# Kernel tuning notes

Measured on AMD Instinct MI355X. Metric: run time of the kernel, lower is better.

Reference implementation:

```python
import jax, jax.numpy as jnp
import numpy as np
import math

NLAT, NLON, LMAX, MMAX = 512, 1024, 50, 50
CHUNK = 8192  # grid chunk for brute-force 3-NN (keeps dist matrix ~134MB)


def _cc_nodes_weights(n):
    """Clenshaw-Curtis nodes theta_j = pi*j/(n-1) and weights for int_{-1}^{1} f(cos t)."""
    N = n - 1
    t = np.pi * np.arange(n) / N
    K = N // 2
    k = np.arange(1, K + 1)
    b = np.where(2 * k == N, 1.0, 2.0)
    S = np.cos(2.0 * np.outer(t, k)) @ (b / (4.0 * k ** 2 - 1.0))
    c = np.full(n, 2.0); c[0] = c[-1] = 1.0
    w = (c / N) * (1.0 - S)
    return t, w


def _legendre(lmax, mmax, theta):
    """Orthonormalized associated Legendre P[l, m, j] = N_lm P_l^m(cos theta_j)."""
    ct, st = np.cos(theta), np.sin(theta)
    P = np.zeros((lmax, mmax, theta.shape[0]))
    P[0, 0] = math.sqrt(1.0 / (4.0 * math.pi))
    for m in range(1, mmax):
        P[m, m] = -math.sqrt((2 * m + 1) / (2.0 * m)) * st * P[m - 1, m - 1]
    for m in range(mmax):
        if m + 1 < lmax:
            P[m + 1, m] = math.sqrt(2 * m + 3) * ct * P[m, m]
        for l in range(m + 2, lmax):
            a = math.sqrt((4.0 * l * l - 1.0) / (l * l - m * m))
            bb = math.sqrt(((l - 1.0) ** 2 - m * m) / (4.0 * (l - 1.0) ** 2 - 1.0))
            P[l, m] = a * (ct * P[l - 1, m] - bb * P[l - 2, m])
    return P

_THETA, _WQ_np = _cc_nodes_weights(NLAT)
_PLM = jnp.asarray(_legendre(LMAX, MMAX, _THETA), jnp.float32)   # (lmax, mmax, nlat)
_WQ = jnp.asarray(_WQ_np, jnp.float32)                            # (nlat,)

# equiangular target grid from __init__: theta in [0, pi), phi in [-pi, pi)
_gi, _gj = np.meshgrid(np.arange(0, 512), np.arange(-512, 512), indexing='ij')
_GRID = jnp.asarray(np.stack([_gi.ravel(), _gj.ravel()], -1).astype(np.float32) / 512.0 * np.pi)  # (M, 2)


def to_spherical(coords):
    """coords (B,N,3) -> (r (B,N), angles (B,N,2)) with azimuth already shifted by -pi."""
    x, y, z = coords[..., 0], coords[..., 1], coords[..., 2]
    r = jnp.sqrt(x * x + y * y + z * z)
    nyz = jnp.sqrt(y * y + z * z)          # tril-norm chain reduces to (r, ||(y,z)||, |z|)
    phi1 = jnp.arccos(x / r)
    base = jnp.arccos(y / nyz)
    phi2 = jnp.where(z < 0, 2.0 * jnp.pi - base, base)
    sph = jnp.stack([phi1, phi2 - jnp.pi], -1)  # forward() subtracts pi from azimuth
    return r, sph


def three_nn(grid, pts):
    """grid (M,2), pts (B,N,2) -> squared dists (B,M,3), idx (B,M,3) of 3 nearest cloud points."""
    gch = grid.reshape(-1, CHUNK, 2)

    def per_batch(p):
        def f(g):
            d2 = jnp.sum((g[:, None, :] - p[None, :, :]) ** 2, -1)  # (CHUNK, N)
            nd, idx = jax.lax.top_k(-d2, 3)
            return -nd, idx
        d, i = jax.lax.map(f, gch)
        return d.reshape(-1, 3), i.reshape(-1, 3)

    return jax.vmap(per_batch)(pts)


def real_sht(f):
    """f (B, nlat, nlon) -> complex coeffs (B, lmax, mmax)."""
    F = jnp.fft.rfft(f, axis=-1)[:, :, :MMAX] * (2.0 * jnp.pi / NLON)  # (B, nlat, mmax)
    Fw = F * _WQ[None, :, None]
    return jnp.einsum('bkm,lmk->blm', Fw, _PLM)


def _branch(pc):
    r, sph = to_spherical(pc)
    dist, idx = three_nn(_GRID, sph)
    w = dist / jnp.sum(dist, -1, keepdims=True)                  # faithful: dist/sum, not 1/dist
    rg = jax.vmap(lambda rr, ii: rr[ii])(r, idx)                 # (B, M, 3)
    interp = jnp.sum(rg * w, -1).reshape(-1, NLAT, NLON)
    return real_sht(interp)


def setup_inputs() -> dict:
    key = jax.random.key(0)
    k1, k2 = jax.random.split(key)
    pred = jax.random.normal(k1, (2, 2048, 3), dtype=jnp.float32)
    target = jax.random.normal(k2, (2, 2048, 3), dtype=jnp.float32)
    return {"pred": pred, "target": target}


def reference(pred, target):
    cp = _branch(pred)
    ct = _branch(target)
    return jnp.mean((cp.real - ct.real) ** 2)
```

## Files before the change

### kernel.cpp

```cpp
#include <hip/hip_runtime.h>
#include <math.h>

#define NLAT 512
#define NLON 1024
#define LMAX 50
#define MMAX 50
#define NPTS 2048
#define NIMG 4
#define M_GRID (NLAT * NLON)

#define NBT 32
#define NBP 64
#define NBINS (NBT * NBP)
#define NPAIR (2 * LMAX * MMAX)
#define NTRI  (LMAX * (LMAX + 1) / 2)

#define PI_F     3.14159274101257324e0f
#define TWO_PI_F 6.28318548202514648e0f
#define WB       (PI_F / 32.0f)
#define INV_WB   (32.0f / PI_F)

__global__ __launch_bounds__(256) void k_setup_bin(const float* __restrict__ pred,
                                                   const float* __restrict__ targ,
                                                   float* __restrict__ wq,
                                                   double* __restrict__ costab,
                                                   float* __restrict__ plm,
                                                   float4* __restrict__ spts_g,
                                                   unsigned short* __restrict__ bstart_g,
                                                   double* __restrict__ acc,
                                                   int* __restrict__ counter) {
    if (blockIdx.x < 128) {
        int tid = blockIdx.x * 256 + threadIdx.x;
        if (tid == 0) { acc[0] = 0.0; counter[0] = 0; }

        {
            int j = blockIdx.x * 4 + (threadIdx.x >> 6);
            int lane = threadIdx.x & 63;
            double t = M_PI * (double)j / 511.0;
            double S = 0.0;
            for (int k = lane + 1; k <= 255; k += 64) {
                S += cos(2.0 * t * (double)k) * (2.0 / (4.0 * (double)k * k - 1.0));
            }
            for (int off = 32; off > 0; off >>= 1) S += __shfl_down(S, off);
            if (lane == 0) {
                double c = (j == 0 || j == 511) ? 1.0 : 2.0;
                wq[j] = (float)((c / 511.0) * (1.0 - S));
            }
        }
        if (tid < 1024) {
            costab[tid] = cos(2.0 * M_PI * (double)tid / 1024.0);
        }
        if (blockIdx.x < 100) {
            __shared__ double fa[MMAX];
            __shared__ double al[LMAX], bl[LMAX];
            int m = blockIdx.x >> 1;
            int t = threadIdx.x;
            if (t >= 1 && t < MMAX) {
                fa[t] = -sqrt((2.0 * t + 1.0) / (2.0 * t));
            }
            if (t >= m + 2 && t < LMAX) {
                double ll = (double)t, mm = (double)m, lm1 = (double)(t - 1);
                al[t] = sqrt((4.0 * ll * ll - 1.0) / (ll * ll - mm * mm));
                bl[t] = sqrt((lm1 * lm1 - mm * mm) / (4.0 * lm1 * lm1 - 1.0));
            }
            __syncthreads();
            int k = ((blockIdx.x & 1) << 8) + t;
            double theta = M_PI * (double)k / 511.0;
            double ct = cos(theta), st = sin(theta);
            double pmm = sqrt(1.0 / (4.0 * M_PI));
            for (int i = 1; i <= m; ++i) {
                pmm = fa[i] * st * pmm;
            }
            plm[((size_t)m * MMAX + m) * 512 + k] = (float)pmm;
            if (m + 1 < LMAX) {
                double pm1 = sqrt(2.0 * m + 3.0) * ct * pmm;
                plm[((size_t)(m + 1) * MMAX + m) * 512 + k] = (float)pm1;
                double pm2 = pmm;
                for (int l = m + 2; l < LMAX; ++l) {
                    double p = al[l] * (ct * pm1 - bl[l] * pm2);
                    plm[((size_t)l * MMAX + m) * 512 + k] = (float)p;
                    pm2 = pm1; pm1 = p;
                }
            }
        }
        return;
    }

    int img = blockIdx.x - 128;
    int branch = img >> 1, b = img & 1;
    const float* src = (branch ? targ : pred) + (size_t)b * NPTS * 3;
    __shared__ float sth[NPTS], sphi[NPTS], srr[NPTS];
    __shared__ int cnt[NBINS];
    __shared__ int bstart[NBINS];
    __shared__ int partial[256];
    __shared__ int binid[NPTS];
    int tid = threadIdx.x;

    for (int i = tid; i < NBINS; i += 256) cnt[i] = 0;
    for (int i = tid; i < NPTS; i += 256) {
        float x = src[3 * i], y = src[3 * i + 1], z = src[3 * i + 2];
        float r = sqrtf(x * x + y * y + z * z);
        float nyz = sqrtf(y * y + z * z);
        float phi1 = acosf(x / r);
        float base = acosf(y / nyz);
        float phi2 = (z < 0.0f) ? (TWO_PI_F - base) : base;
        sth[i] = phi1; sphi[i] = phi2 - PI_F; srr[i] = r;
    }
    __syncthreads();
    for (int i = tid; i < NPTS; i += 256) {
        int bt = min(max((int)(sth[i] * INV_WB), 0), NBT - 1);
        int bp = min(max((int)((sphi[i] + PI_F) * INV_WB), 0), NBP - 1);
        int bn = bt * NBP + bp;
        binid[i] = bn;
        atomicAdd(&cnt[bn], 1);
    }
    __syncthreads();
    int base = tid * 8, s = 0;
    #pragma unroll
    for (int j = 0; j < 8; ++j) s += cnt[base + j];
    partial[tid] = s;
    __syncthreads();
    for (int offs = 1; offs < 256; offs <<= 1) {
        int v = (tid >= offs) ? partial[tid - offs] : 0;
        __syncthreads();
        partial[tid] += v;
        __syncthreads();
    }
    int run = (tid == 0) ? 0 : partial[tid - 1];
    #pragma unroll
    for (int j = 0; j < 8; ++j) { bstart[base + j] = run; run += cnt[base + j]; }
    __syncthreads();
    unsigned short* bsg = bstart_g + (size_t)img * (NBINS + 1);
    for (int i = tid; i < NBINS; i += 256) {
        bsg[i] = (unsigned short)bstart[i];
        cnt[i] = bstart[i];
    }
    if (tid == 0) bsg[NBINS] = (unsigned short)NPTS;
    __syncthreads();
    float4* sg = spts_g + (size_t)img * NPTS;
    for (int i = tid; i < NPTS; i += 256) {
        int bn = binid[i];
        int pos = atomicAdd(&cnt[bn], 1);
        sg[pos] = make_float4(sth[i], sphi[i], srr[i], 0.0f);
    }
}

struct Top3 {
    float d0, d1, d2, r0, r1, r2;
    __device__ void init() { d0 = d1 = d2 = 1e30f; r0 = r1 = r2 = 0.0f; }
    __device__ void ins(float d, float rv) {
        bool c2 = d < d2, c1 = d < d1, c0 = d < d0;
        d2 = c1 ? d1 : (c2 ? d : d2);   r2 = c1 ? r1 : (c2 ? rv : r2);
        d1 = c0 ? d0 : (c1 ? d : d1);   r1 = c0 ? r0 : (c1 ? rv : r1);
        d0 = c0 ? d : d0;               r0 = c0 ? rv : r0;
    }
    __device__ float out() const {
        return (d0 * r0 + d1 * r1 + d2 * r2) / (d0 + d1 + d2);
    }
};

__global__ __launch_bounds__(512, 4) void k_nn(const float4* __restrict__ spts_g,
                                               const unsigned short* __restrict__ bstart_g,
                                               float* __restrict__ interp) {
    __shared__ float4 spts[NPTS];
    __shared__ unsigned short sstart[NBINS + 1];
    int bid = blockIdx.x;
    int img = bid >> 8;
    int blk = bid & 255;
    const float4* sg = spts_g + (size_t)img * NPTS;
    const unsigned short* bsg = bstart_g + (size_t)img * (NBINS + 1);
    int tid = threadIdx.x;
    for (int i = tid; i < NPTS; i += 512) spts[i] = sg[i];
    for (int i = tid; i < NBINS + 1; i += 512) sstart[i] = bsg[i];
    __syncthreads();

    int w = tid >> 6, lane = tid & 63;
    int patch = blk * 8 + w;
    int pi = patch >> 6, pj = patch & 63;
    int qi = lane >> 2, qj0 = (lane & 3) * 4;
    int gi = pi * 16 + qi;
    int gj0 = pj * 16 + qj0;
    float gt  = (float)gi * (1.0f / 512.0f) * PI_F;
    float gp0 = (float)(gj0     - 512) * (1.0f / 512.0f) * PI_F;
    float gp1 = (float)(gj0 + 1 - 512) * (1.0f / 512.0f) * PI_F;
    float gp2 = (float)(gj0 + 2 - 512) * (1.0f / 512.0f) * PI_F;
    float gp3 = (float)(gj0 + 3 - 512) * (1.0f / 512.0f) * PI_F;
    int qbt  = min(max((int)(gt * INV_WB), 0), NBT - 1);
    int qbp0 = min(max((int)((gp0 + PI_F) * INV_WB), 0), NBP - 1);
    int qbp3 = min(max((int)((gp3 + PI_F) * INV_WB), 0), NBP - 1);
    int bt0 = __shfl(qbt, 0), bt1 = __shfl(qbt, 63);
    int bp0 = __shfl(qbp0, 0), bp1 = __shfl(qbp3, 63);

    Top3 qA, qB, qC, qD;
    qA.init(); qB.init(); qC.init(); qD.init();

    auto scan_span = [&](int t, int p0, int p1) {
        int s = sstart[t * NBP + p0], e = sstart[t * NBP + p1 + 1];
        #pragma unroll 2
        for (int i = s; i < e; ++i) {
            float4 pt = spts[i];
            float dx  = gt - pt.x;
            float dxx = dx * dx;
            float dy0 = gp0 - pt.y;
            float dy1 = gp1 - pt.y;
            float dy2 = gp2 - pt.y;
            float dy3 = gp3 - pt.y;
            float dA  = fmaf(dy0, dy0, dxx);
            float dB  = fmaf(dy1, dy1, dxx);
            float dC  = fmaf(dy2, dy2, dxx);
            float dD  = fmaf(dy3, dy3, dxx);
            if (__any(dA < qA.d2 || dB < qB.d2)) {
                qA.ins(dA, pt.z);
                qB.ins(dB, pt.z);
            }
            if (__any(dC < qC.d2 || dD < qD.d2)) {
                qC.ins(dC, pt.z);
                qD.ins(dD, pt.z);
            }
        }
    };

    for (int t = bt0; t <= bt1; ++t) scan_span(t, bp0, bp1);
    for (int r = 1; r <= 70; ++r) {
        if (r >= 2) {
            float bnd = (float)(r - 1) * WB * 0.999f;
            float b2 = bnd * bnd;
            if (__all(b2 > qA.d2 && b2 > qB.d2 && b2 > qC.d2 && b2 > qD.d2)) break;
        }
        int tlo = bt0 - r, thi = bt1 + r, plo = bp0 - r, phi = bp1 + r;
        int cplo = max(plo, 0), cphi = min(phi, NBP - 1);
        if (tlo >= 0)       scan_span(tlo, cplo, cphi);
        if (thi <= NBT - 1) scan_span(thi, cplo, cphi);
        int ctlo = max(tlo + 1, 0), cthi = min(thi - 1, NBT - 1);
        if (plo >= 0)       for (int t = ctlo; t <= cthi; ++t) scan_span(t, plo, plo);
        if (phi <= NBP - 1) for (int t = ctlo; t <= cthi; ++t) scan_span(t, phi, phi);
        if (tlo <= 0 && thi >= NBT - 1 && plo <= 0 && phi >= NBP - 1) break;
    }
    float4 outv = make_float4(qA.out(), qB.out(), qC.out(), qD.out());
    *(float4*)&interp[(size_t)img * M_GRID + (size_t)gi * NLON + gj0] = outv;
}

__global__ __launch_bounds__(512) void k_dft(const float* __restrict__ interp,
                                             const double* __restrict__ costab,
                                             const float* __restrict__ wq,
                                             double* __restrict__ ediff) {
    __shared__ double sdf[NLON];
    __shared__ double sct[NLON];
    __shared__ double ge[320];
    __shared__ double go[320];
    int bid = blockIdx.x;
    int b = bid >> 9, k = bid & 511;
    const float* rowp = interp + (size_t)b * M_GRID + (size_t)k * NLON;
    const float* rowt = interp + (size_t)(2 + b) * M_GRID + (size_t)k * NLON;
    int tid = threadIdx.x;
    for (int i = tid; i < NLON; i += 512) {
        sdf[i] = (double)rowp[i] - (double)rowt[i];
        sct[i] = costab[i];
    }
    __syncthreads();
    if (tid < 320) {
        int n = tid;
        double a = 0.0, c = 0.0;
        if (n == 0) {
            a = sdf[0];
            c = sdf[512];
        } else if (n < 256) {
            a = sdf[n] + sdf[1024 - n];
            c = sdf[512 - n] + sdf[512 + n];
        } else if (n == 256) {
            a = sdf[256] + sdf[768];
            c = 0.0;
        }
        ge[n] = a + c;
        go[n] = a - c;
    }
    __syncthreads();
    double scale = (double)wq[k] * (6.283185307179586 / 1024.0);
    int w = tid >> 6, lane = tid & 63;
    const double* gp = (w & 1) ? go : ge;
    for (int m = w; m < MMAX; m += 8) {
        double c  = sct[(m * lane) & 1023];
        double s  = sct[(m * lane + 768) & 1023];
        double cd = sct[(m * 64) & 1023];
        double sd = sct[(m * 64 + 768) & 1023];
        double a = 0.0;
        #pragma unroll
        for (int i = 0; i < 5; ++i) {
            int n = lane + (i << 6);
            a = fma(gp[n], c, a);
            double cn = fma(cd, c, -(sd * s));
            double sn = fma(cd, s, sd * c);
            c = cn; s = sn;
        }
        #pragma unroll
        for (int off = 32; off > 0; off >>= 1) a += __shfl_xor(a, off);
        if (lane == 0) {
            ediff[((size_t)b * MMAX + m) * 512 + k] = a * scale;
        }
    }
}

__global__ __launch_bounds__(256) void k_loss(const double* __restrict__ ediff,
                                              const float* __restrict__ plm,
                                              double* __restrict__ acc,
                                              int* __restrict__ counter,
                                              float* __restrict__ out) {
    int tid = threadIdx.x;
    int gtid = blockIdx.x * 256 + tid;
    int triple = gtid >> 4, j = gtid & 15;
    double c = 0.0;
    int valid = (triple < 2 * NTRI);
    {
        int b = triple / NTRI;
        int p = triple % NTRI;
        int l = (int)((sqrtf(8.0f * (float)p + 1.0f) - 1.0f) * 0.5f);
        while ((l + 1) * (l + 2) / 2 <= p) ++l;
        while (l * (l + 1) / 2 > p) --l;
        int m = p - l * (l + 1) / 2;
        if (valid) {
            const double* E = ediff + ((size_t)b * MMAX + m) * 512;
            const float*  P = plm + ((size_t)l * MMAX + m) * 512;
            for (int i = 0; i < 32; ++i) {
                int k = j + (i << 4);
                c = fma((double)P[k], E[k], c);
            }
        }
    }
    c += __shfl_xor(c, 1);
    c += __shfl_xor(c, 2);
    c += __shfl_xor(c, 4);
    c += __shfl_xor(c, 8);
    __shared__ double red[16];
    if (j == 0) red[tid >> 4] = valid ? c * c : 0.0;
    __syncthreads();
    if (tid == 0) {
        double s = 0.0;
        for (int i = 0; i < 16; ++i) s += red[i];
        atomicAdd(acc, s);
        __threadfence();
        int old = atomicAdd(counter, 1);
        if (old == (int)gridDim.x - 1) {
            double tot = atomicAdd(acc, 0.0);
            out[0] = (float)(tot / (double)NPAIR);
        }
    }
}

extern "C" void kernel_launch(void* const* d_in, const int* in_sizes, int n_in,
                              void* d_out, int out_size, void* d_ws, size_t ws_size,
                              hipStream_t stream) {
    const float* pred = (const float*)d_in[0];
    const float* targ = (const float*)d_in[1];

    char* ws = (char*)d_ws;
    size_t off = 0;
    auto alloc = [&](size_t bytes) -> void* {
        void* p = ws + off;
        off = (off + bytes + 255) & ~(size_t)255;
        return p;
    };
    float*  wq      = (float*) alloc(512 * sizeof(float));
    double* costab  = (double*)alloc(1024 * sizeof(double));
    float*  plm     = (float*) alloc((size_t)LMAX * MMAX * 512 * sizeof(float));
    float4* spts    = (float4*)alloc((size_t)NIMG * NPTS * sizeof(float4));
    unsigned short* bstart = (unsigned short*)alloc((size_t)NIMG * (NBINS + 1) * sizeof(unsigned short));
    float*  interp  = (float*) alloc((size_t)NIMG * M_GRID * sizeof(float));
    double* ediff   = (double*)alloc((size_t)2 * MMAX * 512 * sizeof(double));
    double* acc     = (double*)alloc(sizeof(double));
    int*    counter = (int*)   alloc(sizeof(int));
    (void)ws_size; (void)in_sizes; (void)n_in; (void)out_size;

    k_setup_bin<<<132, 256, 0, stream>>>(pred, targ, wq, costab, plm, spts, bstart,
                                         acc, counter);
    k_nn<<<NIMG * 256, 512, 0, stream>>>(spts, bstart, interp);
    k_dft<<<2 * 512, 512, 0, stream>>>(interp, costab, wq, ediff);
    int nb = (2 * NTRI * 16 + 255) / 256;
    k_loss<<<nb, 256, 0, stream>>>(ediff, plm, acc, counter, (float*)d_out);
}
```

Before: 107.0 us.

## Refine spatial binning grid and keep per-point data in registers during binning

Doubles the bin resolution in both theta and phi, so each bin holds fewer points. This should cut the candidate points the nearest-neighbour kernel scans per grid cell, but the ring search may now need more rings and more bin lookups. The setup kernel keeps per-point angles, radius and bin id in registers instead of shared arrays. It also pads the count array to avoid bank conflicts and fuses the bin-start writes into the prefix-scan pass, which removes a sync and some shared memory.

Result: slower. 116.7 us (+9.1%).

```diff
diff --git a/kernel.cpp b/kernel.cpp
--- a/kernel.cpp
+++ b/kernel.cpp
@@ -9,16 +9,19 @@
 #define NIMG 4
 #define M_GRID (NLAT * NLON)
 
-#define NBT 32
-#define NBP 64
+#define NBT 64
+#define NBP 128
 #define NBINS (NBT * NBP)
 #define NPAIR (2 * LMAX * MMAX)
 #define NTRI  (LMAX * (LMAX + 1) / 2)
 
 #define PI_F     3.14159274101257324e0f
 #define TWO_PI_F 6.28318548202514648e0f
-#define WB       (PI_F / 32.0f)
-#define INV_WB   (32.0f / PI_F)
+#define WB       (PI_F / 64.0f)
+#define INV_WB   (64.0f / PI_F)
+
+#define CNTI(b) ((b) + ((b) >> 5))
+#define CNT_WORDS (NBINS + (NBINS >> 5))
 
 __global__ __launch_bounds__(256) void k_setup_bin(const float* __restrict__ pred,
                                                    const float* __restrict__ targ,
@@ -89,35 +92,33 @@
     int img = blockIdx.x - 128;
     int branch = img >> 1, b = img & 1;
     const float* src = (branch ? targ : pred) + (size_t)b * NPTS * 3;
-    __shared__ float sth[NPTS], sphi[NPTS], srr[NPTS];
-    __shared__ int cnt[NBINS];
-    __shared__ int bstart[NBINS];
+    __shared__ int cnt[CNT_WORDS];
     __shared__ int partial[256];
-    __shared__ int binid[NPTS];
     int tid = threadIdx.x;
 
-    for (int i = tid; i < NBINS; i += 256) cnt[i] = 0;
-    for (int i = tid; i < NPTS; i += 256) {
+    for (int i = tid; i < CNT_WORDS; i += 256) cnt[i] = 0;
+    float th[8], ph[8], rr[8];
+    int   bn[8];
+    __syncthreads();
+    #pragma unroll
+    for (int j = 0; j < 8; ++j) {
+        int i = tid + (j << 8);
         float x = src[3 * i], y = src[3 * i + 1], z = src[3 * i + 2];
         float r = sqrtf(x * x + y * y + z * z);
         float nyz = sqrtf(y * y + z * z);
         float phi1 = acosf(x / r);
         float base = acosf(y / nyz);
         float phi2 = (z < 0.0f) ? (TWO_PI_F - base) : base;
-        sth[i] = phi1; sphi[i] = phi2 - PI_F; srr[i] = r;
-    }
-    __syncthreads();
-    for (int i = tid; i < NPTS; i += 256) {
-        int bt = min(max((int)(sth[i] * INV_WB), 0), NBT - 1);
-        int bp = min(max((int)((sphi[i] + PI_F) * INV_WB), 0), NBP - 1);
-        int bn = bt * NBP + bp;
-        binid[i] = bn;
-        atomicAdd(&cnt[bn], 1);
-    }
-    __syncthreads();
-    int base = tid * 8, s = 0;
+        th[j] = phi1; ph[j] = phi2 - PI_F; rr[j] = r;
+        int bt = min(max((int)(th[j] * INV_WB), 0), NBT - 1);
+        int bp = min(max((int)((ph[j] + PI_F) * INV_WB), 0), NBP - 1);
+        bn[j] = bt * NBP + bp;
+        atomicAdd(&cnt[CNTI(bn[j])], 1);
+    }
+    __syncthreads();
+    int base = tid * 32, s = 0;
     #pragma unroll
-    for (int j = 0; j < 8; ++j) s += cnt[base + j];
+    for (int j = 0; j < 32; ++j) s += cnt[CNTI(base + j)];
     partial[tid] = s;
     __syncthreads();
     for (int offs = 1; offs < 256; offs <<= 1) {
@@ -126,22 +127,23 @@
         partial[tid] += v;
         __syncthreads();
     }
+    unsigned short* bsg = bstart_g + (size_t)img * (NBINS + 1);
     int run = (tid == 0) ? 0 : partial[tid - 1];
     #pragma unroll
-    for (int j = 0; j < 8; ++j) { bstart[base + j] = run; run += cnt[base + j]; }
-    __syncthreads();
-    unsigned short* bsg = bstart_g + (size_t)img * (NBINS + 1);
-    for (int i = tid; i < NBINS; i += 256) {
-        bsg[i] = (unsigned short)bstart[i];
-        cnt[i] = bstart[i];
+    for (int j = 0; j < 32; ++j) {
+        int bb = base + j;
+        int v = cnt[CNTI(bb)];
+        cnt[CNTI(bb)] = run;
+        bsg[bb] = (unsigned short)run;
+        run += v;
     }
     if (tid == 0) bsg[NBINS] = (unsigned short)NPTS;
     __syncthreads();
     float4* sg = spts_g + (size_t)img * NPTS;
-    for (int i = tid; i < NPTS; i += 256) {
-        int bn = binid[i];
-        int pos = atomicAdd(&cnt[bn], 1);
-        sg[pos] = make_float4(sth[i], sphi[i], srr[i], 0.0f);
+    #pragma unroll
+    for (int j = 0; j < 8; ++j) {
+        int pos = atomicAdd(&cnt[CNTI(bn[j])], 1);
+        sg[pos] = make_float4(th[j], ph[j], rr[j], 0.0f);
     }
 }
 
@@ -221,7 +223,7 @@
     };
 
     for (int t = bt0; t <= bt1; ++t) scan_span(t, bp0, bp1);
-    for (int r = 1; r <= 70; ++r) {
+    for (int r = 1; r <= 150; ++r) {
         if (r >= 2) {
             float bnd = (float)(r - 1) * WB * 0.999f;
             float b2 = bnd * bnd;
```
